# Optimization experiments

Hardware: AMD Instinct MI355X
Metric: run time of the kernel (lower is better)

The kernel has to match this reference:

```python
import jax, jax.numpy as jnp
import numpy as np

B, L, D_IN, H, N, D_OUT = 32, 4096, 32, 256, 32, 16  # N = d_state//2 (conjugate pairs)


def setup_inputs() -> dict:
    key = jax.random.key(0)
    ks = jax.random.split(key, 16)
    s = lambda *sh: 1.0 / np.sqrt(sh[0])
    inp = {
        'data': jax.random.normal(ks[0], (B, L, D_IN), jnp.float32),
        # input projector: Linear(D_IN, H//2) -> ReLU -> Linear(H//2, H)
        'w1': jax.random.normal(ks[1], (D_IN, H // 2), jnp.float32) * s(D_IN),
        'b1': jnp.zeros((H // 2,), jnp.float32),
        'w2': jax.random.normal(ks[2], (H // 2, H), jnp.float32) * s(H // 2),
        'b2': jnp.zeros((H,), jnp.float32),
        # S4D diagonal SSM kernel params
        'log_dt': jax.random.uniform(ks[3], (H,), jnp.float32,
                                     np.log(0.001), np.log(0.1)),
        'A_re': -0.5 * jnp.ones((H, N), jnp.float32),
        'A_im': jnp.broadcast_to(np.pi * jnp.arange(N, dtype=jnp.float32), (H, N)),
        'C_re': jax.random.normal(ks[4], (H, N), jnp.float32) * s(2),
        'C_im': jax.random.normal(ks[5], (H, N), jnp.float32) * s(2),
        'D': jax.random.normal(ks[6], (H,), jnp.float32),
        # S4Block output position-wise linear H -> 2H with GLU
        'Wg': jax.random.normal(ks[7], (H, 2 * H), jnp.float32) * s(H),
        'bg': jnp.zeros((2 * H,), jnp.float32),
        # output projector: Linear(H, H//2) -> ReLU -> Linear(H//2, D_OUT)
        'w3': jax.random.normal(ks[8], (H, H // 2), jnp.float32) * s(H),
        'b3': jnp.zeros((H // 2,), jnp.float32),
        'w4': jax.random.normal(ks[9], (H // 2, D_OUT), jnp.float32) * s(H // 2),
        'b4': jnp.zeros((D_OUT,), jnp.float32),
    }
    return inp


def _s4_forward(data, w1, b1, w2, b2, log_dt, A_re, A_im, C_re, C_im, D,
                Wg, bg, w3, b3, w4, b4):
    # input projector (dropout disabled: eval mode)
    x = jnp.maximum(jnp.dot(data, w1) + b1, 0.0)
    x = jnp.dot(x, w2) + b2                      # (B, L, H)

    u = jnp.transpose(x, (0, 2, 1))              # (B, H, L)
    Lx = u.shape[-1]

    # S4D kernel: k[h,l] = 2 Re( sum_n C (e^{dtA}-1)/A * e^{dtA l} )
    dt = jnp.exp(log_dt)[:, None]                # (H, 1)
    A = A_re + 1j * A_im                         # (H, N)
    dtA = dt * A                                 # (H, N)
    C = C_re + 1j * C_im
    K_coef = C * (jnp.exp(dtA) - 1.0) / A        # (H, N)
    vand = jnp.exp(dtA[:, :, None] * jnp.arange(Lx))   # (H, N, L)
    k = 2.0 * jnp.einsum('hn,hnl->hl', K_coef, vand).real  # (H, L)

    # FFT convolution (causal, via 2L-point FFT) + skip D*u
    nfft = 2 * Lx
    kf = jnp.fft.rfft(k, nfft)                   # (H, nfft//2+1)
    uf = jnp.fft.rfft(u, nfft)                   # (B, H, nfft//2+1)
    y = jnp.fft.irfft(uf * kf[None], nfft)[..., :Lx] + D[None, :, None] * u

    y = jnp.transpose(y, (0, 2, 1))              # (B, L, H)
    y = jax.nn.gelu(y, approximate=False)

    # output linear with GLU
    y = jnp.dot(y, Wg) + bg                      # (B, L, 2H)
    a, b = jnp.split(y, 2, axis=-1)
    y = a * jax.nn.sigmoid(b)                    # (B, L, H)

    last = y[:, -1, :]                           # (B, H)
    z = jnp.maximum(jnp.dot(last, w3) + b3, 0.0)
    return jnp.dot(z, w4) + b4                   # (B, D_OUT); activ_type=None -> identity


def reference(data, w1, b1, w2, b2, log_dt, A_re, A_im, C_re, C_im, D,
              Wg, bg, w3, b3, w4, b4):
    return _s4_forward(data, w1, b1, w2, b2, log_dt, A_re, A_im, C_re, C_im, D,
                       Wg, bg, w3, b3, w4, b4)
```

## Files before the change

### kernel.cpp

```cpp
#include <hip/hip_runtime.h>
#include <math.h>


#define L_LEN 4096
#define H_DIM 256
#define J_DIM 128
#define DIN   32
#define NSTATE 32
#define GRID_PREP 4096

typedef float f32x4 __attribute__((ext_vector_type(4)));
typedef short s16x8 __attribute__((ext_vector_type(8)));

__device__ __forceinline__ short f2bf(float x) {
  union { float f; unsigned u; } a; a.f = x;
  unsigned r = a.u + 0x7fffu + ((a.u >> 16) & 1u);
  return (short)(r >> 16);
}

__global__ __launch_bounds__(256) void k_prep(
    const float* __restrict__ w1, const float* __restrict__ w2,
    const float* __restrict__ log_dt,
    const float* __restrict__ A_re, const float* __restrict__ A_im,
    const float* __restrict__ C_re, const float* __restrict__ C_im,
    float* __restrict__ kkP, float* __restrict__ P,
    short* __restrict__ w1T, short* __restrict__ w2T)
{
  const int bid = blockIdx.x, tid = threadIdx.x;
  __shared__ float kcr[512], kci[512];

  {
    int i = bid * 256 + tid;
    if (i < 8192) {
      P[i] = 0.f;
    } else if (i < 12288) {
      int idx = i - 8192;
      int n = idx >> 5, k = idx & 31;
      w1T[idx] = f2bf(w1[k * J_DIM + n]);
    } else if (i < 45056) {
      int idx = i - 12288;
      int h = idx >> 7, k = idx & 127;
      w2T[idx] = f2bf(w2[k * H_DIM + h]);
    }
  }

  const int hg = bid >> 8, lc = bid & 255;
  for (int e = tid; e < 512; e += 256) {
    int n = e & 31, h2 = e >> 5;
    int h = hg * 16 + h2;
    float dt = expf(log_dt[h]);
    float are = A_re[h * NSTATE + n], aim = A_im[h * NSTATE + n];
    float dr = dt * are, di = dt * aim;
    float ed = expf(dr);
    float c, s; sincosf(di, &s, &c);
    float nr = ed * c - 1.f, ni = ed * s;
    float d2 = are * are + aim * aim;
    float qr = (nr * are + ni * aim) / d2;
    float qi = (ni * are - nr * aim) / d2;
    float cr = C_re[h * NSTATE + n], ci = C_im[h * NSTATE + n];
    kcr[n * 16 + h2] = cr * qr - ci * qi;
    kci[n * 16 + h2] = cr * qi + ci * qr;
  }
  __syncthreads();

  {
    int hh = tid & 15, lw = tid >> 4;
    int h = hg * 16 + hh, l = lc * 16 + lw;
    float fm = (float)((L_LEN - 1) - l);
    float dt = expf(log_dt[h]);
    float ar  = A_re[h * NSTATE];
    float aib = A_im[h * NSTATE + 1];
    float mag = expf(dt * ar * fm);
    float th = dt * aib * fm;
    float s1, c1; sincosf(th, &s1, &c1);
    float cn = 1.f, sn = 0.f, acc = 0.f;
#pragma unroll
    for (int n = 0; n < NSTATE; n++) {
      acc += kcr[n * 16 + hh] * cn - kci[n * 16 + hh] * sn;
      float c2 = cn * c1 - sn * s1;
      sn = sn * c1 + cn * s1;
      cn = c2;
    }
    float val = 2.f * mag * acc;
    int c  = l >> 6, rt = (l >> 4) & 3, q = (l >> 2) & 3, r = l & 3;
    int w  = h >> 6, ht = (h >> 4) & 3, s15 = h & 15;
    kkP[((((c * 4 + w) * 4 + ht) * 4 + rt) * 64 + q * 16 + s15) * 4 + r] = val;
  }
}

__global__ __launch_bounds__(256) void k_main(
    const float* __restrict__ data, const float* __restrict__ b1v,
    const float* __restrict__ b2v, const float* __restrict__ Dv,
    const short* __restrict__ w1T, const short* __restrict__ w2T,
    const float* __restrict__ kkP, float* __restrict__ P)
{
  const int bidx = blockIdx.x, tid = threadIdx.x;
  const int wave = tid >> 6, lane = tid & 63;
  const int quad = lane >> 4, l15 = lane & 15;
  const int b  = bidx >> 6;
  const int l0 = (bidx & 63) * 64;

  __shared__ short x1s[64 * 136];

  {
    const float* dp = data + ((size_t)b * L_LEN + (size_t)(l0 + wave * 16 + l15)) * DIN + quad * 8;
    f32x4 d0 = *(const f32x4*)dp;
    f32x4 d1 = *(const f32x4*)(dp + 4);
    s16x8 af;
    af[0] = f2bf(d0[0]); af[1] = f2bf(d0[1]); af[2] = f2bf(d0[2]); af[3] = f2bf(d0[3]);
    af[4] = f2bf(d1[0]); af[5] = f2bf(d1[1]); af[6] = f2bf(d1[2]); af[7] = f2bf(d1[3]);
#pragma unroll
    for (int c = 0; c < 8; c++) {
      s16x8 bf = *(const s16x8*)(w1T + (c * 16 + l15) * DIN + quad * 8);
      f32x4 a0 = {0.f, 0.f, 0.f, 0.f};
      a0 = __builtin_amdgcn_mfma_f32_16x16x32_bf16(af, bf, a0, 0, 0, 0);
      float bb = b1v[c * 16 + l15];
#pragma unroll
      for (int r = 0; r < 4; r++) {
        float v = fmaxf(a0[r] + bb, 0.f);
        x1s[(wave * 16 + quad * 4 + r) * 136 + c * 16 + l15] = f2bf(v);
      }
    }
  }

  s16x8 wf[4][4];
#pragma unroll
  for (int ht = 0; ht < 4; ht++)
#pragma unroll
    for (int ks = 0; ks < 4; ks++)
      wf[ht][ks] = *(const s16x8*)(w2T + (wave * 64 + ht * 16 + l15) * J_DIM + ks * 32 + quad * 8);

  __syncthreads();

  f32x4 acc[4][4];
#pragma unroll
  for (int rt = 0; rt < 4; rt++)
#pragma unroll
    for (int ht = 0; ht < 4; ht++)
      acc[rt][ht] = (f32x4){0.f, 0.f, 0.f, 0.f};

#pragma unroll
  for (int ks = 0; ks < 4; ks++) {
#pragma unroll
    for (int rt = 0; rt < 4; rt++) {
      s16x8 af = *(const s16x8*)&x1s[(rt * 16 + l15) * 136 + ks * 32 + quad * 8];
#pragma unroll
      for (int ht = 0; ht < 4; ht++)
        acc[rt][ht] = __builtin_amdgcn_mfma_f32_16x16x32_bf16(af, wf[ht][ks], acc[rt][ht], 0, 0, 0);
    }
  }

#pragma unroll
  for (int ht = 0; ht < 4; ht++) {
    int h = wave * 64 + ht * 16 + l15;
    float b2h = b2v[h], Dh = Dv[h];
    const f32x4* kp = ((const f32x4*)kkP)
                    + ((((l0 >> 6) * 4 + wave) * 4 + ht) * 4) * 64 + lane;
    float s = 0.f;
#pragma unroll
    for (int rt = 0; rt < 4; rt++) {
      f32x4 kv = kp[rt * 64];
#pragma unroll
      for (int r = 0; r < 4; r++) {
        int l = l0 + rt * 16 + quad * 4 + r;
        float uu = acc[rt][ht][r] + b2h;
        s = fmaf(kv[r], uu, s);
        if (l == L_LEN - 1) s = fmaf(Dh, uu, s);
      }
    }
    s += __shfl_xor(s, 16, 64);
    s += __shfl_xor(s, 32, 64);
    if (quad == 0) atomicAdd(&P[b * H_DIM + h], s);
  }
}

__global__ __launch_bounds__(1024) void k_tail(
    const float* __restrict__ P, const float* __restrict__ Wg,
    const float* __restrict__ bgv, const float* __restrict__ w3,
    const float* __restrict__ b3v, const float* __restrict__ w4,
    const float* __restrict__ b4v, float* __restrict__ out)
{
  const int b = blockIdx.x, t = threadIdx.x;
  __shared__ float g[H_DIM];
  __shared__ float part[2][512];
  __shared__ float glu[H_DIM];
  __shared__ float zp[8][J_DIM];
  __shared__ float zf[J_DIM];

  if (t < H_DIM) {
    float p = P[b * H_DIM + t];
    g[t] = 0.5f * p * (1.f + erff(p * 0.70710678118654752f));
  }
  __syncthreads();

  {
    int col = t & 511, kc = t >> 9;
    const float* wp = Wg + (size_t)(kc * 128) * 512 + col;
    float acc = 0.f;
#pragma unroll 16
    for (int j = 0; j < 128; j++)
      acc = fmaf(g[kc * 128 + j], wp[(size_t)j * 512], acc);
    part[kc][col] = acc;
  }
  __syncthreads();
  if (t < 512) part[0][t] = bgv[t] + part[0][t] + part[1][t];
  __syncthreads();
  if (t < H_DIM)
    glu[t] = part[0][t] * (1.f / (1.f + expf(-part[0][H_DIM + t])));
  __syncthreads();

  {
    int col = t & 127, kc = t >> 7;
    const float* wp = w3 + (size_t)(kc * 32) * J_DIM + col;
    float acc = 0.f;
#pragma unroll
    for (int j = 0; j < 32; j++)
      acc = fmaf(glu[kc * 32 + j], wp[(size_t)j * J_DIM], acc);
    zp[kc][col] = acc;
  }
  __syncthreads();
  if (t < J_DIM) {
    float s = b3v[t];
#pragma unroll
    for (int k = 0; k < 8; k++) s += zp[k][t];
    zf[t] = fmaxf(s, 0.f);
  }
  __syncthreads();

  if (t < 16) {
    float s = b4v[t];
#pragma unroll
    for (int i = 0; i < J_DIM; i++)
      s = fmaf(zf[i], w4[i * 16 + t], s);
    out[b * 16 + t] = s;
  }
}

extern "C" void kernel_launch(void* const* d_in, const int* in_sizes, int n_in,
                              void* d_out, int out_size, void* d_ws, size_t ws_size,
                              hipStream_t stream)
{
  const float* data   = (const float*)d_in[0];
  const float* w1     = (const float*)d_in[1];
  const float* b1v    = (const float*)d_in[2];
  const float* w2     = (const float*)d_in[3];
  const float* b2v    = (const float*)d_in[4];
  const float* log_dt = (const float*)d_in[5];
  const float* A_re   = (const float*)d_in[6];
  const float* A_im   = (const float*)d_in[7];
  const float* C_re   = (const float*)d_in[8];
  const float* C_im   = (const float*)d_in[9];
  const float* Dv     = (const float*)d_in[10];
  const float* Wg     = (const float*)d_in[11];
  const float* bgv    = (const float*)d_in[12];
  const float* w3     = (const float*)d_in[13];
  const float* b3v    = (const float*)d_in[14];
  const float* w4     = (const float*)d_in[15];
  const float* b4v    = (const float*)d_in[16];
  float* outp = (float*)d_out;

  char* ws = (char*)d_ws;
  float* kkP = (float*)ws;
  float* P   = (float*)(ws + 4194304);
  short* w1T = (short*)(ws + 4194304 + 32768);
  short* w2T = (short*)(ws + 4194304 + 40960);

  k_prep<<<GRID_PREP, 256, 0, stream>>>(w1, w2, log_dt, A_re, A_im, C_re, C_im,
                                        kkP, P, w1T, w2T);
  k_main<<<2048, 256, 0, stream>>>(data, b1v, b2v, Dv, w1T, w2T, kkP, P);
  k_tail<<<32, 1024, 0, stream>>>(P, Wg, bgv, w3, b3v, w4, b4v, outp);
}
```

Measured before the change: 146.9 us.

## Loop four batches per block and replace atomics with partial-sum buffer

k_main now launches 512 blocks, and each block handles four batch elements for one L chunk. The w2 fragments in registers are loaded once and reused across those batches. Atomic accumulation into P is replaced by per-chunk partial sums written to a buffer, which k_tail reduces over the 64 chunks. This also drops the P zeroing from k_prep. The trade-offs are less grid parallelism in k_main, serialized batch iterations with extra syncs, and a larger workspace for the partials.

```diff
diff --git a/kernel.cpp b/kernel.cpp
--- a/kernel.cpp
+++ b/kernel.cpp
@@ -23,7 +23,7 @@
     const float* __restrict__ log_dt,
     const float* __restrict__ A_re, const float* __restrict__ A_im,
     const float* __restrict__ C_re, const float* __restrict__ C_im,
-    float* __restrict__ kkP, float* __restrict__ P,
+    float* __restrict__ kkP,
     short* __restrict__ w1T, short* __restrict__ w2T)
 {
   const int bid = blockIdx.x, tid = threadIdx.x;
@@ -31,14 +31,11 @@
 
   {
     int i = bid * 256 + tid;
-    if (i < 8192) {
-      P[i] = 0.f;
-    } else if (i < 12288) {
-      int idx = i - 8192;
-      int n = idx >> 5, k = idx & 31;
-      w1T[idx] = f2bf(w1[k * J_DIM + n]);
-    } else if (i < 45056) {
-      int idx = i - 12288;
+    if (i < 4096) {
+      int n = i >> 5, k = i & 31;
+      w1T[i] = f2bf(w1[k * J_DIM + n]);
+    } else if (i < 36864) {
+      int idx = i - 4096;
       int h = idx >> 7, k = idx & 127;
       w2T[idx] = f2bf(w2[k * H_DIM + h]);
     }
@@ -92,36 +89,15 @@
     const float* __restrict__ data, const float* __restrict__ b1v,
     const float* __restrict__ b2v, const float* __restrict__ Dv,
     const short* __restrict__ w1T, const short* __restrict__ w2T,
-    const float* __restrict__ kkP, float* __restrict__ P)
+    const float* __restrict__ kkP, float* __restrict__ Pp)
 {
   const int bidx = blockIdx.x, tid = threadIdx.x;
   const int wave = tid >> 6, lane = tid & 63;
   const int quad = lane >> 4, l15 = lane & 15;
-  const int b  = bidx >> 6;
-  const int l0 = (bidx & 63) * 64;
+  const int lc = bidx & 63, bg = bidx >> 6;
+  const int l0 = lc * 64;
 
   __shared__ short x1s[64 * 136];
-
-  {
-    const float* dp = data + ((size_t)b * L_LEN + (size_t)(l0 + wave * 16 + l15)) * DIN + quad * 8;
-    f32x4 d0 = *(const f32x4*)dp;
-    f32x4 d1 = *(const f32x4*)(dp + 4);
-    s16x8 af;
-    af[0] = f2bf(d0[0]); af[1] = f2bf(d0[1]); af[2] = f2bf(d0[2]); af[3] = f2bf(d0[3]);
-    af[4] = f2bf(d1[0]); af[5] = f2bf(d1[1]); af[6] = f2bf(d1[2]); af[7] = f2bf(d1[3]);
-#pragma unroll
-    for (int c = 0; c < 8; c++) {
-      s16x8 bf = *(const s16x8*)(w1T + (c * 16 + l15) * DIN + quad * 8);
-      f32x4 a0 = {0.f, 0.f, 0.f, 0.f};
-      a0 = __builtin_amdgcn_mfma_f32_16x16x32_bf16(af, bf, a0, 0, 0, 0);
-      float bb = b1v[c * 16 + l15];
-#pragma unroll
-      for (int r = 0; r < 4; r++) {
-        float v = fmaxf(a0[r] + bb, 0.f);
-        x1s[(wave * 16 + quad * 4 + r) * 136 + c * 16 + l15] = f2bf(v);
-      }
-    }
-  }
 
   s16x8 wf[4][4];
 #pragma unroll
@@ -130,65 +106,103 @@
     for (int ks = 0; ks < 4; ks++)
       wf[ht][ks] = *(const s16x8*)(w2T + (wave * 64 + ht * 16 + l15) * J_DIM + ks * 32 + quad * 8);
 
-  __syncthreads();
-
-  f32x4 acc[4][4];
-#pragma unroll
-  for (int rt = 0; rt < 4; rt++)
-#pragma unroll
-    for (int ht = 0; ht < 4; ht++)
-      acc[rt][ht] = (f32x4){0.f, 0.f, 0.f, 0.f};
-
-#pragma unroll
-  for (int ks = 0; ks < 4; ks++) {
-#pragma unroll
-    for (int rt = 0; rt < 4; rt++) {
-      s16x8 af = *(const s16x8*)&x1s[(rt * 16 + l15) * 136 + ks * 32 + quad * 8];
+
+#pragma unroll 1
+  for (int bb = 0; bb < 4; bb++) {
+    const int b = bg * 4 + bb;
+
+    __syncthreads();
+
+    {
+      const float* dp = data + ((size_t)b * L_LEN + (size_t)(l0 + wave * 16 + l15)) * DIN + quad * 8;
+      f32x4 d0 = *(const f32x4*)dp;
+      f32x4 d1 = *(const f32x4*)(dp + 4);
+      s16x8 af;
+      af[0] = f2bf(d0[0]); af[1] = f2bf(d0[1]); af[2] = f2bf(d0[2]); af[3] = f2bf(d0[3]);
+      af[4] = f2bf(d1[0]); af[5] = f2bf(d1[1]); af[6] = f2bf(d1[2]); af[7] = f2bf(d1[3]);
+#pragma unroll
+      for (int c = 0; c < 8; c++) {
+        s16x8 bf = *(const s16x8*)(w1T + (c * 16 + l15) * DIN + quad * 8);
+        f32x4 a0 = {0.f, 0.f, 0.f, 0.f};
+        a0 = __builtin_amdgcn_mfma_f32_16x16x32_bf16(af, bf, a0, 0, 0, 0);
+        float bbi = b1v[c * 16 + l15];
+#pragma unroll
+        for (int r = 0; r < 4; r++) {
+          float v = fmaxf(a0[r] + bbi, 0.f);
+          x1s[(wave * 16 + quad * 4 + r) * 136 + c * 16 + l15] = f2bf(v);
+        }
+      }
+    }
+    __syncthreads();
+
+    f32x4 acc[4][4];
+#pragma unroll
+    for (int rt = 0; rt < 4; rt++)
 #pragma unroll
       for (int ht = 0; ht < 4; ht++)
-        acc[rt][ht] = __builtin_amdgcn_mfma_f32_16x16x32_bf16(af, wf[ht][ks], acc[rt][ht], 0, 0, 0);
-    }
-  }
-
-#pragma unroll
-  for (int ht = 0; ht < 4; ht++) {
-    int h = wave * 64 + ht * 16 + l15;
-    float b2h = b2v[h], Dh = Dv[h];
-    const f32x4* kp = ((const f32x4*)kkP)
-                    + ((((l0 >> 6) * 4 + wave) * 4 + ht) * 4) * 64 + lane;
-    float s = 0.f;
-#pragma unroll
-    for (int rt = 0; rt < 4; rt++) {
-      f32x4 kv = kp[rt * 64];
-#pragma unroll
-      for (int r = 0; r < 4; r++) {
-        int l = l0 + rt * 16 + quad * 4 + r;
-        float uu = acc[rt][ht][r] + b2h;
-        s = fmaf(kv[r], uu, s);
-        if (l == L_LEN - 1) s = fmaf(Dh, uu, s);
+        acc[rt][ht] = (f32x4){0.f, 0.f, 0.f, 0.f};
+
+#pragma unroll
+    for (int ks = 0; ks < 4; ks++) {
+#pragma unroll
+      for (int rt = 0; rt < 4; rt++) {
+        s16x8 af = *(const s16x8*)&x1s[(rt * 16 + l15) * 136 + ks * 32 + quad * 8];
+#pragma unroll
+        for (int ht = 0; ht < 4; ht++)
+          acc[rt][ht] = __builtin_amdgcn_mfma_f32_16x16x32_bf16(af, wf[ht][ks], acc[rt][ht], 0, 0, 0);
       }
     }
-    s += __shfl_xor(s, 16, 64);
-    s += __shfl_xor(s, 32, 64);
-    if (quad == 0) atomicAdd(&P[b * H_DIM + h], s);
+
+#pragma unroll
+    for (int ht = 0; ht < 4; ht++) {
+      int h = wave * 64 + ht * 16 + l15;
+      float b2h = b2v[h], Dh = Dv[h];
+      const f32x4* kp = ((const f32x4*)kkP)
+                      + (((lc * 4 + wave) * 4 + ht) * 4) * 64 + lane;
+      float s = 0.f;
+#pragma unroll
+      for (int rt = 0; rt < 4; rt++) {
+        f32x4 kv = kp[rt * 64];
+#pragma unroll
+        for (int r = 0; r < 4; r++) {
+          int l = l0 + rt * 16 + quad * 4 + r;
+          float uu = acc[rt][ht][r] + b2h;
+          s = fmaf(kv[r], uu, s);
+          if (l == L_LEN - 1) s = fmaf(Dh, uu, s);
+        }
+      }
+      s += __shfl_xor(s, 16, 64);
+      s += __shfl_xor(s, 32, 64);
+      if (quad == 0) Pp[(size_t)(lc * 32 + b) * H_DIM + h] = s;
+    }
   }
 }
 
 __global__ __launch_bounds__(1024) void k_tail(
-    const float* __restrict__ P, const float* __restrict__ Wg,
+    const float* __restrict__ Pp, const float* __restrict__ Wg,
     const float* __restrict__ bgv, const float* __restrict__ w3,
     const float* __restrict__ b3v, const float* __restrict__ w4,
     const float* __restrict__ b4v, float* __restrict__ out)
 {
   const int b = blockIdx.x, t = threadIdx.x;
+  __shared__ float pp[4][H_DIM];
   __shared__ float g[H_DIM];
   __shared__ float part[2][512];
   __shared__ float glu[H_DIM];
   __shared__ float zp[8][J_DIM];
   __shared__ float zf[J_DIM];
 
+  {
+    int h = t & 255, kc = t >> 8;
+    float s = 0.f;
+#pragma unroll
+    for (int i = 0; i < 16; i++)
+      s += Pp[(size_t)((kc * 16 + i) * 32 + b) * H_DIM + h];
+    pp[kc][h] = s;
+  }
+  __syncthreads();
   if (t < H_DIM) {
-    float p = P[b * H_DIM + t];
+    float p = pp[0][t] + pp[1][t] + pp[2][t] + pp[3][t];
     g[t] = 0.5f * p * (1.f + erff(p * 0.70710678118654752f));
   }
   __syncthreads();
@@ -261,12 +275,12 @@
 
   char* ws = (char*)d_ws;
   float* kkP = (float*)ws;
-  float* P   = (float*)(ws + 4194304);
-  short* w1T = (short*)(ws + 4194304 + 32768);
-  short* w2T = (short*)(ws + 4194304 + 40960);
+  float* Pp  = (float*)(ws + 4194304);
+  short* w1T = (short*)(ws + 4194304 + 2097152);
+  short* w2T = (short*)(ws + 4194304 + 2097152 + 8192);
 
   k_prep<<<GRID_PREP, 256, 0, stream>>>(w1, w2, log_dt, A_re, A_im, C_re, C_im,
-                                        kkP, P, w1T, w2T);
-  k_main<<<2048, 256, 0, stream>>>(data, b1v, b2v, Dv, w1T, w2T, kkP, P);
-  k_tail<<<32, 1024, 0, stream>>>(P, Wg, bgv, w3, b3v, w4, b4v, outp);
-}
+                                        kkP, w1T, w2T);
+  k_main<<<512, 256, 0, stream>>>(data, b1v, b2v, Dv, w1T, w2T, kkP, Pp);
+  k_tail<<<32, 1024, 0, stream>>>(Pp, Wg, bgv, w3, b3v, w4, b4v, outp);
+}
```

After: 142.7 us. 1.03x faster.
